# Kernel optimization log

Measured on AMD Instinct MI355X. Metric: run time of the kernel, lower is better.

The kernel has to match this reference:

```python
import jax, jax.numpy as jnp
import numpy as np

NUM_CLASSES = 4
EPS = 1e-8
LAMBDA_CREDA = 1.0
LAMBDA_ENTROPY = 0.1


def setup_inputs() -> dict:
    key = jax.random.key(0)
    k1, k2, k3, k4, k5 = jax.random.split(key, 5)
    Ns, Nt, D, C = 1024, 1024, 2048, NUM_CLASSES
    return {
        "features_s": jax.random.normal(k1, (Ns, D), jnp.float32),
        "logits_s": jax.random.normal(k2, (Ns, C), jnp.float32),
        "labels_s": jax.random.randint(k3, (Ns,), 0, C),
        "features_t": jax.random.normal(k4, (Nt, D), jnp.float32),
        "logits_t": jax.random.normal(k5, (Nt, C), jnp.float32),
    }


def _sq_cdist(x, y):
    # squared euclidean pairwise distances, [n, m]
    x2 = jnp.sum(x * x, axis=1)
    y2 = jnp.sum(y * y, axis=1)
    return jnp.maximum(x2[:, None] + y2[None, :] - 2.0 * (x @ y.T), 0.0)


def _h2(K):
    # Renyi quadratic entropy: -log2(tr(A @ A)), A = K / tr(K).
    # tr(A @ A) == sum(A * A.T), avoiding the full matmul.
    tr = jnp.trace(K) + EPS
    A = K / tr
    return -jnp.log2(jnp.sum(A * A.T) + EPS)


def reference(features_s, logits_s, labels_s, features_t, logits_t):
    C = NUM_CLASSES
    # classification loss (mean cross entropy)
    logp = jax.nn.log_softmax(logits_s, axis=1)
    loss_cls = -jnp.mean(jnp.take_along_axis(logp, labels_s[:, None], axis=1))
    # target entropy loss
    probs_t = jax.nn.softmax(logits_t, axis=1)
    ent_per = -jnp.sum(probs_t * jnp.log(probs_t + EPS), axis=1)  # [Nt]
    loss_ent = jnp.mean(ent_per)
    pseudo = jnp.argmax(jax.lax.stop_gradient(probs_t), axis=1)  # [Nt]
    max_ent = jnp.log(jnp.float32(C))
    w = 1.0 - ent_per / (max_ent + EPS)  # uncertainty weights, [Nt]

    Ns = features_s.shape[0]
    comb = jnp.concatenate([features_s, features_t], axis=0)  # [N, D]
    D2 = _sq_cdist(comb, comb)  # [N, N], shared across classes
    N = D2.shape[0]
    triu = jnp.triu(jnp.ones((N, N), bool), 1)

    def per_class(c):
        m_s = labels_s == c  # [Ns]
        m_t = pseudo == c    # [Nt]
        valid = (jnp.sum(m_s) >= 2) & (jnp.sum(m_t) >= 2)
        m = jnp.concatenate([m_s, m_t])  # [N]
        # median heuristic over off-diagonal pairs within the class subset
        pm = triu & m[:, None] & m[None, :]
        cnt = jnp.sum(pm)
        dv = jnp.where(pm, D2, jnp.inf)
        med = jnp.sort(dv.ravel())[jnp.maximum((cnt - 1) // 2, 0)]  # lower median (torch.median)
        med = jnp.where(cnt > 0, med, jnp.float32(1.0))
        sigma_sq = med + 1e-6  # sigma = sqrt(med + 1e-6)
        K = jnp.exp(-D2 / (2.0 * sigma_sq + EPS))  # [N, N]
        ms = m_s.astype(K.dtype)
        mt = m_t.astype(K.dtype)
        vt = mt * w  # uncertainty-weighted target mask
        # masked kernel blocks (rows/cols outside the class are zero -> same traces as gathered submatrices)
        Kss = K[:Ns, :Ns] * (ms[:, None] * ms[None, :])
        Ktt = K[Ns:, Ns:] * (vt[:, None] * vt[None, :])
        Kst = K[:Ns, Ns:] * (ms[:, None] * mt[None, :])
        Kmix = jnp.concatenate(
            [jnp.concatenate([Kss, Kst], axis=1), jnp.concatenate([Kst.T, Ktt], axis=1)],
            axis=0,
        )
        term = _h2(Kmix) - 0.5 * (_h2(Kss) + _h2(Ktt))
        return jnp.where(valid, term, jnp.float32(0.0)), valid

    terms, valids = jax.vmap(per_class)(jnp.arange(C))
    nvalid = jnp.sum(valids)
    loss_creda = jnp.where(
        nvalid > 0, jnp.sum(terms) / jnp.maximum(nvalid, 1).astype(terms.dtype), jnp.float32(0.0)
    )
    return loss_cls + LAMBDA_CREDA * loss_creda + LAMBDA_ENTROPY * loss_ent
```

## Files before the change

### kernel.cpp

```cpp
#include <hip/hip_runtime.h>
#include <math.h>

#define EPSF 1e-8f
#define NSRC 1024
#define NTGT 1024
#define NTOT 2048
#define DIM  2048
#define NCLS 4

typedef __attribute__((ext_vector_type(8))) short short8v;
typedef __attribute__((ext_vector_type(4))) float f32x4;

constexpr size_t OFF_D2      = 0;
constexpr size_t OFF_WBUF    = (size_t)NTOT * NTOT * 4;
constexpr size_t OFF_NORMS   = OFF_WBUF + 1024 * 4;
constexpr size_t OFF_CLSOF   = OFF_NORMS + 2048 * 4;
constexpr size_t OFF_CIDX    = OFF_CLSOF + 2048 * 4;
constexpr size_t OFF_CCNT    = OFF_CIDX + 4 * 2048 * 4;
constexpr size_t OFF_CNS     = OFF_CCNT + 16;
constexpr size_t OFF_CNT     = OFF_CNS + 16;
constexpr size_t OFF_LOSS2   = OFF_CNT + 16;
constexpr size_t OFF_SEL1    = OFF_LOSS2 + 16;
constexpr size_t OFF_SEL2    = OFF_SEL1 + 16;
constexpr size_t OFF_SELBASE = OFF_SEL2 + 16;
constexpr size_t OFF_INV2S   = OFF_SELBASE + 16;
constexpr size_t OFF_SSUM    = OFF_INV2S + 16;
constexpr size_t OFF_HIST    = ((OFF_SSUM + 80 + 255) / 256) * 256;
constexpr size_t WS_END      = OFF_HIST + 3 * NCLS * 4096 * 4;

__device__ __forceinline__ float waveReduceSum(float v) {
#pragma unroll
    for (int o = 32; o > 0; o >>= 1) v += __shfl_down(v, o, 64);
    return v;
}

__device__ __forceinline__ short bf16_rne(float x) {
    unsigned u = __float_as_uint(x);
    unsigned r = (u + 0x7FFFu + ((u >> 16) & 1u)) >> 16;
    return (short)r;
}
__device__ __forceinline__ float bf16_to_f32(short h) {
    return __uint_as_float(((unsigned)(unsigned short)h) << 16);
}

__global__ __launch_bounds__(256) void k_norms(const float* __restrict__ fs,
                                               const float* __restrict__ ft,
                                               float* __restrict__ norms) {
    int row = blockIdx.x;
    const float* src = row < NSRC ? fs + (size_t)row * DIM : ft + (size_t)(row - NSRC) * DIM;
    float s = 0.f;
    for (int k = threadIdx.x; k < DIM; k += 256) {
        float v = src[k];
        s = fmaf(v, v, s);
    }
    s = waveReduceSum(s);
    __shared__ float ls[4];
    int lane = threadIdx.x & 63, w = threadIdx.x >> 6;
    if (lane == 0) ls[w] = s;
    __syncthreads();
    if (threadIdx.x == 0) norms[row] = ls[0] + ls[1] + ls[2] + ls[3];
}

__global__ __launch_bounds__(256) void k_rowstats(const float* __restrict__ logits_s,
                                                  const int* __restrict__ labels,
                                                  const float* __restrict__ logits_t,
                                                  float* __restrict__ wbuf,
                                                  int* __restrict__ clsof,
                                                  int* __restrict__ cidx,
                                                  int* __restrict__ ccnt,
                                                  int* __restrict__ cns,
                                                  int* __restrict__ cnt_,
                                                  float* __restrict__ loss2) {
    int tid = blockIdx.x * 256 + threadIdx.x;
    if (tid < NSRC) {
        float4 l = *(const float4*)(logits_s + (size_t)tid * 4);
        float m = fmaxf(fmaxf(l.x, l.y), fmaxf(l.z, l.w));
        float e0 = expf(l.x - m), e1 = expf(l.y - m), e2 = expf(l.z - m), e3 = expf(l.w - m);
        float lse = m + logf(e0 + e1 + e2 + e3);
        int lab = labels[tid];
        float lv = (lab == 0) ? l.x : (lab == 1) ? l.y : (lab == 2) ? l.z : l.w;
        atomicAdd(&loss2[0], lse - lv);
        clsof[tid] = lab;
        atomicAdd(&cns[lab], 1);
        int pos = atomicAdd(&ccnt[lab], 1);
        cidx[lab * NTOT + pos] = tid;
    } else if (tid < NTOT) {
        int j = tid - NSRC;
        float4 l = *(const float4*)(logits_t + (size_t)j * 4);
        float m = fmaxf(fmaxf(l.x, l.y), fmaxf(l.z, l.w));
        float e0 = expf(l.x - m), e1 = expf(l.y - m), e2 = expf(l.z - m), e3 = expf(l.w - m);
        float s = e0 + e1 + e2 + e3;
        float p0 = e0 / s, p1 = e1 / s, p2 = e2 / s, p3 = e3 / s;
        float ent = 0.f;
        ent -= p0 * logf(p0 + EPSF);
        ent -= p1 * logf(p1 + EPSF);
        ent -= p2 * logf(p2 + EPSF);
        ent -= p3 * logf(p3 + EPSF);
        int bi = 0;
        float bv = l.x;
        if (l.y > bv) { bv = l.y; bi = 1; }
        if (l.z > bv) { bv = l.z; bi = 2; }
        if (l.w > bv) { bv = l.w; bi = 3; }
        float w = 1.f - ent / (logf(4.f) + EPSF);
        wbuf[j] = w;
        clsof[tid] = bi;
        atomicAdd(&loss2[1], ent);
        atomicAdd(&cnt_[bi], 1);
        int pos = atomicAdd(&ccnt[bi], 1);
        cidx[bi * NTOT + pos] = tid;
    }
}

__global__ __launch_bounds__(256) void k_gemm_d2(const float* __restrict__ fs,
                                                 const float* __restrict__ ft,
                                                 const float* __restrict__ norms,
                                                 float* __restrict__ D2) {
    __shared__ short Ah[64][40], Al[64][40], Bh[64][40], Bl[64][40];
    int t = threadIdx.x;
    int p = blockIdx.x, by = 0;
    while (p >= 32 - by) { p -= 32 - by; ++by; }
    int bx = by + p;
    int rb = by * 64, cb = bx * 64;

    int sr = t >> 2, sc = (t & 3) * 8;
    int arow = rb + sr, brow = cb + sr;
    const float* asrc = (arow < NSRC ? fs + (size_t)arow * DIM : ft + (size_t)(arow - NSRC) * DIM) + sc;
    const float* bsrc = (brow < NSRC ? fs + (size_t)brow * DIM : ft + (size_t)(brow - NSRC) * DIM) + sc;

    int lane = t & 63;
    int q = lane >> 4;
    int lr = lane & 15;
    int wid = t >> 6;
    int wr = wid >> 1, wc = wid & 1;

    f32x4 acc[2][2] = {};

    for (int k0 = 0; k0 < DIM; k0 += 32) {
        __syncthreads();
        {
            float4 v0 = *(const float4*)(asrc + k0);
            float4 v1 = *(const float4*)(asrc + k0 + 4);
            short8v h, l;
            float vv[8] = {v0.x, v0.y, v0.z, v0.w, v1.x, v1.y, v1.z, v1.w};
#pragma unroll
            for (int i = 0; i < 8; ++i) {
                short hb = bf16_rne(vv[i]);
                h[i] = hb;
                l[i] = bf16_rne(vv[i] - bf16_to_f32(hb));
            }
            *(short8v*)&Ah[sr][sc] = h;
            *(short8v*)&Al[sr][sc] = l;
            v0 = *(const float4*)(bsrc + k0);
            v1 = *(const float4*)(bsrc + k0 + 4);
            float uu[8] = {v0.x, v0.y, v0.z, v0.w, v1.x, v1.y, v1.z, v1.w};
#pragma unroll
            for (int i = 0; i < 8; ++i) {
                short hb = bf16_rne(uu[i]);
                h[i] = hb;
                l[i] = bf16_rne(uu[i] - bf16_to_f32(hb));
            }
            *(short8v*)&Bh[sr][sc] = h;
            *(short8v*)&Bl[sr][sc] = l;
        }
        __syncthreads();
        short8v ah[2], al[2], bh[2], bl[2];
#pragma unroll
        for (int mi = 0; mi < 2; ++mi) {
            int r = wr * 32 + mi * 16 + lr;
            ah[mi] = *(short8v*)&Ah[r][q * 8];
            al[mi] = *(short8v*)&Al[r][q * 8];
        }
#pragma unroll
        for (int ni = 0; ni < 2; ++ni) {
            int r = wc * 32 + ni * 16 + lr;
            bh[ni] = *(short8v*)&Bh[r][q * 8];
            bl[ni] = *(short8v*)&Bl[r][q * 8];
        }
#pragma unroll
        for (int mi = 0; mi < 2; ++mi)
#pragma unroll
            for (int ni = 0; ni < 2; ++ni) {
                acc[mi][ni] = __builtin_amdgcn_mfma_f32_16x16x32_bf16(ah[mi], bh[ni], acc[mi][ni], 0, 0, 0);
                acc[mi][ni] = __builtin_amdgcn_mfma_f32_16x16x32_bf16(ah[mi], bl[ni], acc[mi][ni], 0, 0, 0);
                acc[mi][ni] = __builtin_amdgcn_mfma_f32_16x16x32_bf16(al[mi], bh[ni], acc[mi][ni], 0, 0, 0);
            }
    }

    bool offdiag = (bx != by);
#pragma unroll
    for (int mi = 0; mi < 2; ++mi)
#pragma unroll
        for (int ni = 0; ni < 2; ++ni)
#pragma unroll
            for (int i = 0; i < 4; ++i) {
                int gi = rb + wr * 32 + mi * 16 + q * 4 + i;
                int gj = cb + wc * 32 + ni * 16 + lr;
                float d = fmaxf(norms[gi] + norms[gj] - 2.f * acc[mi][ni][i], 0.f);
                D2[(size_t)gi * NTOT + gj] = d;
                if (offdiag) D2[(size_t)gj * NTOT + gi] = d;
            }
}

__global__ __launch_bounds__(256) void k_radixpass(const float* __restrict__ D2,
                                                   const int* __restrict__ cidx,
                                                   const int* __restrict__ ccnt,
                                                   const int* __restrict__ clsof,
                                                   unsigned* __restrict__ hist,
                                                   const unsigned* __restrict__ sel1,
                                                   const unsigned* __restrict__ sel2,
                                                   int pass) {
    int c = blockIdx.y;
    int n = ccnt[c];
    if (n < 2) return;
    const int* idx = cidx + c * NTOT;
    unsigned* gh = hist + ((size_t)(pass - 1) * NCLS + c) * 4096;
    __shared__ unsigned lh[4096];
    __shared__ unsigned char lcls[NTOT];
    for (int b = threadIdx.x; b < 4096; b += 256) lh[b] = 0;
    for (int j = threadIdx.x; j < NTOT; j += 256) lcls[j] = (unsigned char)clsof[j];
    __syncthreads();
    unsigned s1 = (pass >= 2) ? sel1[c] : 0u;
    unsigned s2 = (pass >= 3) ? sel2[c] : 0u;
    int lane = threadIdx.x & 63;

    for (int a = blockIdx.x; a < n; a += gridDim.x) {
        int i = idx[a];
        const float* drow = D2 + (size_t)i * NTOT;
        for (int j = i + 1 + threadIdx.x; j < NTOT; j += 256) {
            bool want = (lcls[j] == (unsigned char)c);
            unsigned bin = 0;
            if (want) {
                unsigned bits = __float_as_uint(drow[j]);
                if (pass == 1) {
                    bin = bits >> 20;
                } else if (pass == 2) {
                    want = (bits >> 20) == s1;
                    bin = (bits >> 8) & 0xFFFu;
                } else {
                    want = ((bits >> 20) == s1) && (((bits >> 8) & 0xFFFu) == s2);
                    bin = bits & 0xFFu;
                }
            }
            if (pass == 1) {
                while (__any(want)) {
                    unsigned long long m = __ballot(want);
                    int leader = __ffsll((long long)m) - 1;
                    unsigned lbin = __shfl(bin, leader, 64);
                    bool same = want && (bin == lbin);
                    unsigned long long sm = __ballot(same);
                    if (lane == leader) atomicAdd(&lh[lbin], (unsigned)__popcll(sm));
                    want = want && !same;
                }
            } else {
                if (want) atomicAdd(&lh[bin], 1u);
            }
        }
    }
    __syncthreads();
    for (int b = threadIdx.x; b < 4096; b += 256) {
        unsigned v = lh[b];
        if (v) atomicAdd(gh + b, v);
    }
}

__global__ __launch_bounds__(256) void k_select(const unsigned* __restrict__ hist,
                                                const int* __restrict__ ccnt,
                                                unsigned* __restrict__ sel1,
                                                unsigned* __restrict__ sel2,
                                                unsigned* __restrict__ selbase,
                                                float* __restrict__ inv2s,
                                                int pass) {
    int c = blockIdx.x;
    int t = threadIdx.x;
    long long n = ccnt[c];
    long long P = n * (n - 1) / 2;
    if (P == 0) {
        if (t == 0 && pass == 3) {
            inv2s[c] = 1.f / (2.f * (1.0f + 1e-6f) + EPSF);
        }
        return;
    }
    unsigned target = (unsigned)((P - 1) / 2) + 1u - selbase[c];
    const unsigned* h = hist + ((size_t)(pass - 1) * NCLS + c) * 4096;

    unsigned local = 0;
    int b0 = t * 16;
    for (int b = b0; b < b0 + 16; ++b) local += h[b];
    __shared__ unsigned ls[256];
    __shared__ unsigned sbin;
    ls[t] = local;
    if (t == 0) sbin = 0xFFFFFFFFu;
    __syncthreads();
    unsigned prefix = 0;
    for (int i = 0; i < t; ++i) prefix += ls[i];

    unsigned cum = prefix;
    unsigned fbin = 0xFFFFFFFFu, fbase = 0;
    for (int b = b0; b < b0 + 16; ++b) {
        unsigned hv = h[b];
        if (cum + hv >= target) { fbin = (unsigned)b; fbase = cum; break; }
        cum += hv;
    }
    if (fbin != 0xFFFFFFFFu) atomicMin(&sbin, fbin);
    __syncthreads();
    if (fbin == sbin && fbin != 0xFFFFFFFFu) {
        if (pass == 1) {
            sel1[c] = fbin;
            selbase[c] += fbase;
        } else if (pass == 2) {
            sel2[c] = fbin;
            selbase[c] += fbase;
        } else {
            unsigned bits = (sel1[c] << 20) | (sel2[c] << 8) | fbin;
            float med = __uint_as_float(bits);
            inv2s[c] = 1.f / (2.f * (med + 1e-6f) + EPSF);
        }
    }
}

__global__ __launch_bounds__(256) void k_sums(const float* __restrict__ D2,
                                              const int* __restrict__ cidx,
                                              const int* __restrict__ ccnt,
                                              const float* __restrict__ wbuf,
                                              const float* __restrict__ inv2s,
                                              float* __restrict__ S) {
    int c = blockIdx.y;
    int n = ccnt[c];
    if (n == 0) return;
    const int* idx = cidx + c * NTOT;
    float is2 = inv2s[c];
    float ss = 0.f, tt = 0.f, st = 0.f, trs = 0.f, trt = 0.f;
    for (int a = blockIdx.x; a < n; a += gridDim.x) {
        int i = idx[a];
        bool si = i < NSRC;
        float wi = si ? 1.f : wbuf[i - NSRC];
        const float* drow = D2 + (size_t)i * NTOT;
        for (int b = threadIdx.x; b < n; b += 256) {
            int j = idx[b];
            float d = drow[j];
            float Kv = expf(-d * is2);
            float K2 = Kv * Kv;
            bool sj = j < NSRC;
            if (si && sj) {
                ss += K2;
            } else if (!si && !sj) {
                float ww = wi * wbuf[j - NSRC];
                tt += ww * ww * K2;
            } else {
                st += K2;
            }
            if (i == j) {
                if (si) trs += Kv;
                else trt += wi * wi * Kv;
            }
        }
    }
    ss = waveReduceSum(ss);
    tt = waveReduceSum(tt);
    st = waveReduceSum(st);
    trs = waveReduceSum(trs);
    trt = waveReduceSum(trt);
    __shared__ float red[4][5];
    int lane = threadIdx.x & 63, w = threadIdx.x >> 6;
    if (lane == 0) { red[w][0] = ss; red[w][1] = tt; red[w][2] = st; red[w][3] = trs; red[w][4] = trt; }
    __syncthreads();
    if (threadIdx.x < 5) {
        float v = red[0][threadIdx.x] + red[1][threadIdx.x] + red[2][threadIdx.x] + red[3][threadIdx.x];
        atomicAdd(&S[c * 5 + threadIdx.x], v);
    }
}

__global__ void k_final(const float* __restrict__ S,
                        const int* __restrict__ cns,
                        const int* __restrict__ cnt_,
                        const float* __restrict__ loss2,
                        float* __restrict__ out) {
    if (threadIdx.x != 0 || blockIdx.x != 0) return;
    float csum = 0.f;
    int nv = 0;
    for (int c = 0; c < NCLS; ++c) {
        float Sss = S[c * 5 + 0], Stt = S[c * 5 + 1], Sst2 = S[c * 5 + 2];
        float Tss = S[c * 5 + 3], Ttt = S[c * 5 + 4];
        float trs = Tss + EPSF, trt = Ttt + EPSF, trm = Tss + Ttt + EPSF;
        float h2s = -log2f(Sss / (trs * trs) + EPSF);
        float h2t = -log2f(Stt / (trt * trt) + EPSF);
        float h2m = -log2f((Sss + Stt + Sst2) / (trm * trm) + EPSF);
        if (cns[c] >= 2 && cnt_[c] >= 2) {
            csum += h2m - 0.5f * (h2s + h2t);
            nv++;
        }
    }
    float creda = (nv > 0) ? csum / (float)nv : 0.f;
    out[0] = loss2[0] * (1.f / 1024.f) + creda + 0.1f * (loss2[1] * (1.f / 1024.f));
}

extern "C" void kernel_launch(void* const* d_in, const int* in_sizes, int n_in,
                              void* d_out, int out_size, void* d_ws, size_t ws_size,
                              hipStream_t stream) {
    const float* fs  = (const float*)d_in[0];
    const float* ls  = (const float*)d_in[1];
    const int*   lab = (const int*)d_in[2];
    const float* ft  = (const float*)d_in[3];
    const float* lt  = (const float*)d_in[4];
    float* out = (float*)d_out;
    char* ws = (char*)d_ws;

    float*    D2      = (float*)(ws + OFF_D2);
    float*    wbuf    = (float*)(ws + OFF_WBUF);
    float*    norms   = (float*)(ws + OFF_NORMS);
    int*      clsof   = (int*)(ws + OFF_CLSOF);
    int*      cidx    = (int*)(ws + OFF_CIDX);
    int*      ccnt    = (int*)(ws + OFF_CCNT);
    int*      cns     = (int*)(ws + OFF_CNS);
    int*      cnt_    = (int*)(ws + OFF_CNT);
    float*    loss2   = (float*)(ws + OFF_LOSS2);
    unsigned* sel1    = (unsigned*)(ws + OFF_SEL1);
    unsigned* sel2    = (unsigned*)(ws + OFF_SEL2);
    unsigned* selbase = (unsigned*)(ws + OFF_SELBASE);
    float*    inv2s   = (float*)(ws + OFF_INV2S);
    float*    Ssum    = (float*)(ws + OFF_SSUM);
    unsigned* hist    = (unsigned*)(ws + OFF_HIST);

    hipMemsetAsync(ws + OFF_CCNT, 0, WS_END - OFF_CCNT, stream);

    k_norms<<<NTOT, 256, 0, stream>>>(fs, ft, norms);
    k_rowstats<<<NTOT / 256, 256, 0, stream>>>(ls, lab, lt, wbuf, clsof, cidx, ccnt, cns, cnt_, loss2);
    k_gemm_d2<<<528, 256, 0, stream>>>(fs, ft, norms, D2);
    k_radixpass<<<dim3(64, NCLS), 256, 0, stream>>>(D2, cidx, ccnt, clsof, hist, sel1, sel2, 1);
    k_select<<<NCLS, 256, 0, stream>>>(hist, ccnt, sel1, sel2, selbase, inv2s, 1);
    k_radixpass<<<dim3(64, NCLS), 256, 0, stream>>>(D2, cidx, ccnt, clsof, hist, sel1, sel2, 2);
    k_select<<<NCLS, 256, 0, stream>>>(hist, ccnt, sel1, sel2, selbase, inv2s, 2);
    k_radixpass<<<dim3(64, NCLS), 256, 0, stream>>>(D2, cidx, ccnt, clsof, hist, sel1, sel2, 3);
    k_select<<<NCLS, 256, 0, stream>>>(hist, ccnt, sel1, sel2, selbase, inv2s, 3);
    k_sums<<<dim3(64, NCLS), 256, 0, stream>>>(D2, cidx, ccnt, wbuf, inv2s, Ssum);
    k_final<<<1, 64, 0, stream>>>(Ssum, cns, cnt_, loss2, out);
}
```

Measured before the change: 282.9 us.

## Precompute bf16 hi/lo feature split once and feed GEMM from prepacked buffers

Adds a prepass kernel that converts the fp32 features into bf16 high and low planes while computing the row norms. A new GEMM kernel then loads these bf16 planes directly, with a 64-wide K tile and XOR-swizzled shared memory. This removes the repeated per-tile fp32-to-bf16 splitting and halves the global bytes per load in the distance GEMM. In exchange it needs extra workspace and an extra write/read of the split features, and it only runs if the workspace is large enough.

```diff
diff --git a/kernel.cpp b/kernel.cpp
--- a/kernel.cpp
+++ b/kernel.cpp
@@ -27,6 +27,9 @@
 constexpr size_t OFF_SSUM    = OFF_INV2S + 16;
 constexpr size_t OFF_HIST    = ((OFF_SSUM + 80 + 255) / 256) * 256;
 constexpr size_t WS_END      = OFF_HIST + 3 * NCLS * 4096 * 4;
+constexpr size_t OFF_FH      = ((WS_END + 255) / 256) * 256;
+constexpr size_t OFF_FL      = OFF_FH + (size_t)NTOT * DIM * 2;
+constexpr size_t WS_END_PRE  = OFF_FL + (size_t)NTOT * DIM * 2;
 
 __device__ __forceinline__ float waveReduceSum(float v) {
 #pragma unroll
@@ -59,6 +62,36 @@
     if (lane == 0) ls[w] = s;
     __syncthreads();
     if (threadIdx.x == 0) norms[row] = ls[0] + ls[1] + ls[2] + ls[3];
+}
+
+__global__ __launch_bounds__(256) void k_split(const float* __restrict__ fs,
+                                               const float* __restrict__ ft,
+                                               short* __restrict__ Fh,
+                                               short* __restrict__ Fl,
+                                               float* __restrict__ norms) {
+    int row = blockIdx.x;
+    const float* src = row < NSRC ? fs + (size_t)row * DIM : ft + (size_t)(row - NSRC) * DIM;
+    int t = threadIdx.x;
+    float4 v0 = *(const float4*)(src + t * 8);
+    float4 v1 = *(const float4*)(src + t * 8 + 4);
+    float vv[8] = {v0.x, v0.y, v0.z, v0.w, v1.x, v1.y, v1.z, v1.w};
+    short8v h, l;
+    float s = 0.f;
+#pragma unroll
+    for (int i = 0; i < 8; ++i) {
+        s = fmaf(vv[i], vv[i], s);
+        short hb = bf16_rne(vv[i]);
+        h[i] = hb;
+        l[i] = bf16_rne(vv[i] - bf16_to_f32(hb));
+    }
+    *(short8v*)&Fh[(size_t)row * DIM + t * 8] = h;
+    *(short8v*)&Fl[(size_t)row * DIM + t * 8] = l;
+    s = waveReduceSum(s);
+    __shared__ float ls[4];
+    int lane = t & 63, w = t >> 6;
+    if (lane == 0) ls[w] = s;
+    __syncthreads();
+    if (t == 0) norms[row] = ls[0] + ls[1] + ls[2] + ls[3];
 }
 
 __global__ __launch_bounds__(256) void k_rowstats(const float* __restrict__ logits_s,
@@ -111,6 +144,87 @@
     }
 }
 
+__global__ __launch_bounds__(256) void k_gemm_pre(const short* __restrict__ Fh,
+                                                  const short* __restrict__ Fl,
+                                                  const float* __restrict__ norms,
+                                                  float* __restrict__ D2) {
+    __shared__ short LAh[64 * 64], LAl[64 * 64], LBh[64 * 64], LBl[64 * 64];
+    int t = threadIdx.x;
+    int p = blockIdx.x, by = 0;
+    while (p >= 32 - by) { p -= 32 - by; ++by; }
+    int bx = by + p;
+    int rb = by * 64, cb = bx * 64;
+
+    int sr = t >> 2;
+    int c0 = (t & 3) * 2;
+    const short* gAh = Fh + (size_t)(rb + sr) * DIM;
+    const short* gAl = Fl + (size_t)(rb + sr) * DIM;
+    const short* gBh = Fh + (size_t)(cb + sr) * DIM;
+    const short* gBl = Fl + (size_t)(cb + sr) * DIM;
+    int st0 = sr * 64 + ((c0 ^ (sr & 7)) * 8);
+    int st1 = sr * 64 + (((c0 + 1) ^ (sr & 7)) * 8);
+    int go0 = c0 * 8, go1 = (c0 + 1) * 8;
+
+    int lane = t & 63;
+    int q = lane >> 4, lr = lane & 15;
+    int wid = t >> 6, wr = wid >> 1, wc = wid & 1;
+
+    f32x4 acc[2][2] = {};
+
+    for (int k0 = 0; k0 < DIM; k0 += 64) {
+        __syncthreads();
+        *(short8v*)&LAh[st0] = *(const short8v*)(gAh + k0 + go0);
+        *(short8v*)&LAh[st1] = *(const short8v*)(gAh + k0 + go1);
+        *(short8v*)&LAl[st0] = *(const short8v*)(gAl + k0 + go0);
+        *(short8v*)&LAl[st1] = *(const short8v*)(gAl + k0 + go1);
+        *(short8v*)&LBh[st0] = *(const short8v*)(gBh + k0 + go0);
+        *(short8v*)&LBh[st1] = *(const short8v*)(gBh + k0 + go1);
+        *(short8v*)&LBl[st0] = *(const short8v*)(gBl + k0 + go0);
+        *(short8v*)&LBl[st1] = *(const short8v*)(gBl + k0 + go1);
+        __syncthreads();
+#pragma unroll
+        for (int ks = 0; ks < 2; ++ks) {
+            short8v ah[2], al[2], bh[2], bl[2];
+#pragma unroll
+            for (int mi = 0; mi < 2; ++mi) {
+                int r = wr * 32 + mi * 16 + lr;
+                int ch = ((ks * 4 + q) ^ (r & 7)) * 8;
+                ah[mi] = *(short8v*)&LAh[r * 64 + ch];
+                al[mi] = *(short8v*)&LAl[r * 64 + ch];
+            }
+#pragma unroll
+            for (int ni = 0; ni < 2; ++ni) {
+                int r = wc * 32 + ni * 16 + lr;
+                int ch = ((ks * 4 + q) ^ (r & 7)) * 8;
+                bh[ni] = *(short8v*)&LBh[r * 64 + ch];
+                bl[ni] = *(short8v*)&LBl[r * 64 + ch];
+            }
+#pragma unroll
+            for (int mi = 0; mi < 2; ++mi)
+#pragma unroll
+                for (int ni = 0; ni < 2; ++ni) {
+                    acc[mi][ni] = __builtin_amdgcn_mfma_f32_16x16x32_bf16(ah[mi], bh[ni], acc[mi][ni], 0, 0, 0);
+                    acc[mi][ni] = __builtin_amdgcn_mfma_f32_16x16x32_bf16(ah[mi], bl[ni], acc[mi][ni], 0, 0, 0);
+                    acc[mi][ni] = __builtin_amdgcn_mfma_f32_16x16x32_bf16(al[mi], bh[ni], acc[mi][ni], 0, 0, 0);
+                }
+        }
+    }
+
+    bool offdiag = (bx != by);
+#pragma unroll
+    for (int mi = 0; mi < 2; ++mi)
+#pragma unroll
+        for (int ni = 0; ni < 2; ++ni)
+#pragma unroll
+            for (int i = 0; i < 4; ++i) {
+                int gi = rb + wr * 32 + mi * 16 + q * 4 + i;
+                int gj = cb + wc * 32 + ni * 16 + lr;
+                float d = fmaxf(norms[gi] + norms[gj] - 2.f * acc[mi][ni][i], 0.f);
+                D2[(size_t)gi * NTOT + gj] = d;
+                if (offdiag) D2[(size_t)gj * NTOT + gi] = d;
+            }
+}
+
 __global__ __launch_bounds__(256) void k_gemm_d2(const float* __restrict__ fs,
                                                  const float* __restrict__ ft,
                                                  const float* __restrict__ norms,
@@ -420,12 +534,23 @@
     float*    inv2s   = (float*)(ws + OFF_INV2S);
     float*    Ssum    = (float*)(ws + OFF_SSUM);
     unsigned* hist    = (unsigned*)(ws + OFF_HIST);
+    short*    Fh      = (short*)(ws + OFF_FH);
+    short*    Fl      = (short*)(ws + OFF_FL);
 
     hipMemsetAsync(ws + OFF_CCNT, 0, WS_END - OFF_CCNT, stream);
 
-    k_norms<<<NTOT, 256, 0, stream>>>(fs, ft, norms);
+    bool pre = (ws_size >= WS_END_PRE);
+    if (pre) {
+        k_split<<<NTOT, 256, 0, stream>>>(fs, ft, Fh, Fl, norms);
+    } else {
+        k_norms<<<NTOT, 256, 0, stream>>>(fs, ft, norms);
+    }
     k_rowstats<<<NTOT / 256, 256, 0, stream>>>(ls, lab, lt, wbuf, clsof, cidx, ccnt, cns, cnt_, loss2);
-    k_gemm_d2<<<528, 256, 0, stream>>>(fs, ft, norms, D2);
+    if (pre) {
+        k_gemm_pre<<<528, 256, 0, stream>>>(Fh, Fl, norms, D2);
+    } else {
+        k_gemm_d2<<<528, 256, 0, stream>>>(fs, ft, norms, D2);
+    }
     k_radixpass<<<dim3(64, NCLS), 256, 0, stream>>>(D2, cidx, ccnt, clsof, hist, sel1, sel2, 1);
     k_select<<<NCLS, 256, 0, stream>>>(hist, ccnt, sel1, sel2, selbase, inv2s, 1);
     k_radixpass<<<dim3(64, NCLS), 256, 0, stream>>>(D2, cidx, ccnt, clsof, hist, sel1, sel2, 2);
```

Result: faster. 264.3 us (-6.6%).
